# Kernel tuning notes

Measured on AMD Instinct MI355X. Metric: run time of the kernel, lower is better.

## Reference

```python
import jax, jax.numpy as jnp
import numpy as np

B, T, C = 2, 2048, 2048
N_HEADS, N_KV_HEADS = 16, 4
HEAD_DIM = C // N_HEADS  # 128
NUM_GROUPS = N_HEADS // N_KV_HEADS  # 4


def setup_inputs() -> dict:
    key = jax.random.key(0)
    ks = jax.random.split(key, 5)
    s = 1.0 / np.sqrt(C)
    return {
        "x": jax.random.normal(ks[0], (B, T, C), dtype=jnp.float32),
        "Wq": jax.random.normal(ks[1], (C, N_HEADS * HEAD_DIM), dtype=jnp.float32) * s,
        "Wk": jax.random.normal(ks[2], (C, N_KV_HEADS * HEAD_DIM), dtype=jnp.float32) * s,
        "Wv": jax.random.normal(ks[3], (C, N_KV_HEADS * HEAD_DIM), dtype=jnp.float32) * s,
        "Wo": jax.random.normal(ks[4], (C, C), dtype=jnp.float32) * s,
    }


def _rope_tables(seq_len, head_dim, dtype):
    theta = 1.0 / (10000.0 ** (jnp.arange(0, head_dim, 2, dtype=jnp.float32) / head_dim))
    freqs = jnp.arange(seq_len, dtype=jnp.float32)[:, None] * theta[None, :]  # [T, hd/2]
    cos = jnp.concatenate([jnp.cos(freqs), jnp.cos(freqs)], axis=-1)  # [T, hd]
    sin = jnp.concatenate([jnp.sin(freqs), jnp.sin(freqs)], axis=-1)
    return cos.astype(dtype), sin.astype(dtype)


def _rotate_half(x):
    x1, x2 = jnp.split(x, 2, axis=-1)
    return jnp.concatenate([-x2, x1], axis=-1)


def reference(x, Wq, Wk, Wv, Wo):
    b, t, c = x.shape
    q = (x @ Wq).reshape(b, t, N_HEADS, HEAD_DIM).transpose(0, 2, 1, 3)      # [B,H,T,hd]
    k = (x @ Wk).reshape(b, t, N_KV_HEADS, HEAD_DIM).transpose(0, 2, 1, 3)   # [B,Hkv,T,hd]
    v = (x @ Wv).reshape(b, t, N_KV_HEADS, HEAD_DIM).transpose(0, 2, 1, 3)

    cos, sin = _rope_tables(t, HEAD_DIM, x.dtype)  # [T,hd]
    cos = cos[None, None]  # [1,1,T,hd]
    sin = sin[None, None]
    q = q * cos + _rotate_half(q) * sin
    k = k * cos + _rotate_half(k) * sin

    # GQA: expand kv heads (repeat_interleave along head dim)
    k = jnp.repeat(k, NUM_GROUPS, axis=1)  # [B,H,T,hd]
    v = jnp.repeat(v, NUM_GROUPS, axis=1)

    scale = 1.0 / jnp.sqrt(jnp.asarray(HEAD_DIM, dtype=x.dtype))
    scores = jnp.einsum("bhqd,bhkd->bhqk", q, k) * scale  # [B,H,T,T]
    causal = jnp.tril(jnp.ones((t, t), dtype=bool))
    scores = jnp.where(causal[None, None], scores, jnp.asarray(-jnp.inf, dtype=scores.dtype))
    attn = jax.nn.softmax(scores, axis=-1)
    out = jnp.einsum("bhqk,bhkd->bhqd", attn, v)  # [B,H,T,hd]
    out = out.transpose(0, 2, 1, 3).reshape(b, t, c)
    return out @ Wo
```

## Files before the change

kernel.cpp:

```cpp
#include <hip/hip_runtime.h>
#include <hip/hip_bf16.h>
#include <math.h>
#include <utility>

typedef __hip_bfloat16 bf16;
typedef __attribute__((ext_vector_type(8))) short bf16x8;
typedef __attribute__((ext_vector_type(4))) float floatx4;

__device__ __forceinline__ void async_copy16(const bf16* g, bf16* l) {
    __builtin_amdgcn_global_load_lds(
        (__attribute__((address_space(1))) void*)(void*)g,
        (__attribute__((address_space(3))) void*)(void*)l,
        16, 0, 0);
}

__global__ __launch_bounds__(256) void cast_f32_bf16(const float* __restrict__ in,
                                                     bf16* __restrict__ out, int n4) {
    int i = blockIdx.x * 256 + threadIdx.x;
    if (i >= n4) return;
    float4 v = ((const float4*)in)[i];
    union { ushort4 u; bf16 b[4]; } o;
    o.b[0] = __float2bfloat16(v.x);
    o.b[1] = __float2bfloat16(v.y);
    o.b[2] = __float2bfloat16(v.z);
    o.b[3] = __float2bfloat16(v.w);
    ((ushort4*)out)[i] = o.u;
}

__global__ __launch_bounds__(256) void cast_transpose(const float* __restrict__ in,
                                                      bf16* __restrict__ out, int K, int N) {
    __shared__ float tile[32][33];
    int nb = blockIdx.x * 32, kb = blockIdx.y * 32;
    for (int j = threadIdx.y; j < 32; j += 8)
        tile[j][threadIdx.x] = in[(size_t)(kb + j) * N + nb + threadIdx.x];
    __syncthreads();
    for (int j = threadIdx.y; j < 32; j += 8)
        out[(size_t)(nb + j) * K + kb + threadIdx.x] = __float2bfloat16(tile[threadIdx.x][j]);
}

template <bool OUTF32>
__global__ __launch_bounds__(256) void gemm_bt(const bf16* __restrict__ A,
                                               const bf16* __restrict__ Bt,
                                               void* __restrict__ Cout,
                                               int M, int N, int K) {
    __shared__ bf16 As[128 * 32];
    __shared__ bf16 Bs[128 * 32];
    const int tid = threadIdx.x;
    const int wave = tid >> 6, lane = tid & 63;
    const int c = lane & 15, quad = lane >> 4;
    const int wm = wave >> 1, wn = wave & 1;
    const int mBase = blockIdx.y * 128, nBase = blockIdx.x * 128;

    const int sRow = lane >> 2;
    const int sCol = ((lane & 3) ^ ((lane >> 3) & 3)) << 3;
    const int rdOff = (quad ^ ((c >> 1) & 3)) << 3;
    const bf16* gA = A + (size_t)(mBase + wave * 32 + sRow) * K + sCol;
    const bf16* gB = Bt + (size_t)(nBase + wave * 32 + sRow) * K + sCol;
    bf16* lA = As + wave * 1024;
    bf16* lB = Bs + wave * 1024;

    floatx4 acc[4][4];
#pragma unroll
    for (int mt = 0; mt < 4; mt++)
#pragma unroll
        for (int nt = 0; nt < 4; nt++) acc[mt][nt] = (floatx4){0.f, 0.f, 0.f, 0.f};

    for (int k0 = 0; k0 < K; k0 += 32) {
        async_copy16(gA + k0, lA);
        async_copy16(gA + k0 + 16 * K, lA + 512);
        async_copy16(gB + k0, lB);
        async_copy16(gB + k0 + 16 * K, lB + 512);
        __syncthreads();
        bf16x8 af[4], bfr[4];
#pragma unroll
        for (int mt = 0; mt < 4; mt++)
            af[mt] = *(const bf16x8*)(As + (wm * 64 + mt * 16 + c) * 32 + rdOff);
#pragma unroll
        for (int nt = 0; nt < 4; nt++)
            bfr[nt] = *(const bf16x8*)(Bs + (wn * 64 + nt * 16 + c) * 32 + rdOff);
#pragma unroll
        for (int mt = 0; mt < 4; mt++)
#pragma unroll
            for (int nt = 0; nt < 4; nt++)
                acc[mt][nt] = __builtin_amdgcn_mfma_f32_16x16x32_bf16(af[mt], bfr[nt],
                                                                      acc[mt][nt], 0, 0, 0);
        __syncthreads();
    }
#pragma unroll
    for (int mt = 0; mt < 4; mt++)
#pragma unroll
        for (int nt = 0; nt < 4; nt++)
#pragma unroll
            for (int r = 0; r < 4; r++) {
                int row = mBase + wm * 64 + mt * 16 + quad * 4 + r;
                int col = nBase + wn * 64 + nt * 16 + c;
                if (OUTF32)
                    ((float*)Cout)[(size_t)row * N + col] = acc[mt][nt][r];
                else
                    ((bf16*)Cout)[(size_t)row * N + col] = __float2bfloat16(acc[mt][nt][r]);
            }
}

__global__ __launch_bounds__(256) void rope_kernel(bf16* __restrict__ X, int heads, int rowStride) {
    int idx = blockIdx.x * 256 + threadIdx.x;
    int d = idx & 63;
    int h = (idx >> 6) % heads;
    int row = idx / (heads * 64);
    int t = row & 2047;
    float theta = exp2f(-(float)d * 0.20762050593045827f);
    float ang = (float)t * theta;
    float sv, cv;
    __sincosf(ang, &sv, &cv);
    bf16* p = X + (size_t)row * rowStride + h * 128 + d;
    float x1 = __bfloat162float(p[0]);
    float x2 = __bfloat162float(p[64]);
    p[0]  = __float2bfloat16(x1 * cv - x2 * sv);
    p[64] = __float2bfloat16(x2 * cv + x1 * sv);
}

__global__ __launch_bounds__(256) void vtrans(const bf16* __restrict__ QKV,
                                              bf16* __restrict__ Vtg) {
    __shared__ bf16 tile[32][34];
    const int bh = blockIdx.z;
    const int b = bh >> 2, kvh = bh & 3;
    const int t0 = blockIdx.x * 32, d0 = blockIdx.y * 32;
    const bf16* src = QKV + (size_t)b * 2048 * 3072 + 2560 + kvh * 128;
    for (int j = threadIdx.y; j < 32; j += 8)
        tile[j][threadIdx.x] = src[(size_t)(t0 + j) * 3072 + d0 + threadIdx.x];
    __syncthreads();
    bf16* dst = Vtg + (size_t)bh * 128 * 2048;
    for (int j = threadIdx.y; j < 32; j += 8)
        dst[(size_t)(d0 + j) * 2048 + t0 + threadIdx.x] = tile[threadIdx.x][j];
}

__global__ __launch_bounds__(256, 4) void flash_attn3(const bf16* __restrict__ QKV,
                                                      const bf16* __restrict__ Vtg,
                                                      bf16* __restrict__ AO) {
    const int T = 2048, STR = 3072;
    __shared__ bf16 Ks[4 * 64 * 32];
    __shared__ bf16 Vs[2 * 128 * 32];
    __shared__ bf16 Pl[4][16 * 40];
    const int b = blockIdx.z, h = blockIdx.y;
    const int qtile = 31 - blockIdx.x;
    const int q0 = qtile * 64;
    const int kvh = h >> 2;
    const int tid = threadIdx.x, wave = tid >> 6, lane = tid & 63;
    const int c = lane & 15, quad = lane >> 4;
    const float C2 = 0.12751541717525597f;

    const bf16* Kg = QKV + (size_t)b * T * STR + 2048 + kvh * 128;
    const bf16* Vg = Vtg + (size_t)(b * 4 + kvh) * 128 * 2048;
    const int srow = tid >> 2;
    const int xcol = ((tid & 3) ^ ((tid >> 3) & 3)) << 3;
    const int koff = (quad ^ ((c >> 1) & 3)) << 3;
    bf16* PlW = &Pl[wave][0];

    bf16x8 qf[4];
    {
        const bf16* qp = QKV + ((size_t)b * T + q0 + wave * 16 + c) * STR + h * 128 + quad * 8;
#pragma unroll
        for (int ks = 0; ks < 4; ks++) qf[ks] = *(const bf16x8*)(qp + ks * 32);
        const float t = (float)(q0 + wave * 16 + c);
#pragma unroll
        for (int ks = 0; ks < 2; ks++)
#pragma unroll
            for (int j = 0; j < 8; j++) {
                int d = ks * 32 + quad * 8 + j;
                float theta = exp2f((float)d * -0.20762050593045827f);
                float sv, cv;
                __sincosf(t * theta, &sv, &cv);
                float lo = __bfloat162float(((const bf16*)&qf[ks])[j]);
                float hi = __bfloat162float(((const bf16*)&qf[ks + 2])[j]);
                ((bf16*)&qf[ks])[j]     = __float2bfloat16(lo * cv - hi * sv);
                ((bf16*)&qf[ks + 2])[j] = __float2bfloat16(hi * cv + lo * sv);
            }
    }

    floatx4 accO[8];
#pragma unroll
    for (int nt = 0; nt < 8; nt++) accO[nt] = (floatx4){0.f, 0.f, 0.f, 0.f};
    float lrow[4] = {0.f, 0.f, 0.f, 0.f};

    auto tile = [&](int kt0, auto DIAGC) {
        constexpr bool DIAG = decltype(DIAGC)::value;
#pragma unroll
        for (int it = 0; it < 4; it++) {
            async_copy16(Kg + (size_t)(kt0 + srow) * STR + it * 32 + xcol,
                         Ks + it * 2048 + wave * 512);
            async_copy16(Vg + (size_t)((it & 1) * 64 + srow) * 2048 + kt0 + (it >> 1) * 32 + xcol,
                         Vs + it * 2048 + wave * 512);
        }
        __syncthreads();
        floatx4 sf[4];
#pragma unroll
        for (int nt = 0; nt < 4; nt++) sf[nt] = (floatx4){0.f, 0.f, 0.f, 0.f};
#pragma unroll
        for (int ks = 0; ks < 4; ks++)
#pragma unroll
            for (int nt = 0; nt < 4; nt++) {
                bf16x8 kf = *(const bf16x8*)(Ks + ks * 2048 + (nt * 16 + c) * 32 + koff);
                sf[nt] = __builtin_amdgcn_mfma_f32_16x16x32_bf16(qf[ks], kf, sf[nt], 0, 0, 0);
            }
#pragma unroll
        for (int kc = 0; kc < 2; kc++) {
#pragma unroll
            for (int nt2 = 0; nt2 < 2; nt2++) {
                const int nt = kc * 2 + nt2;
#pragma unroll
                for (int r = 0; r < 4; r++) {
                    float p = exp2f(sf[nt][r] * C2);
                    if (DIAG)
                        if (nt * 16 + c > wave * 16 + quad * 4 + r) p = 0.f;
                    lrow[r] += p;
                    PlW[(quad * 4 + r) * 40 + nt2 * 16 + c] = __float2bfloat16(p);
                }
            }
            asm volatile("s_waitcnt lgkmcnt(0)" ::: "memory");
            bf16x8 pf = *(const bf16x8*)(PlW + c * 40 + quad * 8);
#pragma unroll
            for (int nt = 0; nt < 8; nt++) {
                bf16x8 vf = *(const bf16x8*)(Vs + kc * 4096 + (nt * 16 + c) * 32 + koff);
                accO[nt] = __builtin_amdgcn_mfma_f32_16x16x32_bf16(pf, vf, accO[nt], 0, 0, 0);
            }
            asm volatile("" ::: "memory");
        }
        __syncthreads();
    };

    for (int kt0 = 0; kt0 < q0; kt0 += 64)
        tile(kt0, std::integral_constant<bool, false>{});
    tile(q0, std::integral_constant<bool, true>{});

    float inv[4];
#pragma unroll
    for (int r = 0; r < 4; r++) {
        float s = lrow[r];
        s += __shfl_xor(s, 1);
        s += __shfl_xor(s, 2);
        s += __shfl_xor(s, 4);
        s += __shfl_xor(s, 8);
        inv[r] = 1.0f / s;
    }
    const size_t orow = (size_t)b * T + q0 + wave * 16 + quad * 4;
#pragma unroll
    for (int nt = 0; nt < 8; nt++)
#pragma unroll
        for (int r = 0; r < 4; r++)
            AO[(orow + r) * 2048 + h * 128 + nt * 16 + c] =
                __float2bfloat16(accO[nt][r] * inv[r]);
}

extern "C" void kernel_launch(void* const* d_in, const int* in_sizes, int n_in,
                              void* d_out, int out_size, void* d_ws, size_t ws_size,
                              hipStream_t stream) {
    const float* x  = (const float*)d_in[0];
    const float* Wq = (const float*)d_in[1];
    const float* Wk = (const float*)d_in[2];
    const float* Wv = (const float*)d_in[3];
    const float* Wo = (const float*)d_in[4];

    char* ws = (char*)d_ws;
    bf16* xb  = (bf16*)(ws);
    bf16* Vtg = (bf16*)(ws);
    bf16* Wt  = (bf16*)(ws + 16777216);
    bf16* Wot = (bf16*)(ws + 29360128);
    bf16* QKV = (bf16*)(ws + 37748736);
    bf16* AO  = (bf16*)(ws + 62914560);

    cast_f32_bf16<<<8192, 256, 0, stream>>>(x, xb, 2097152);
    cast_transpose<<<dim3(64, 64), dim3(32, 8), 0, stream>>>(Wq, Wt, 2048, 2048);
    cast_transpose<<<dim3(16, 64), dim3(32, 8), 0, stream>>>(Wk, Wt + 2048 * 2048, 2048, 512);
    cast_transpose<<<dim3(16, 64), dim3(32, 8), 0, stream>>>(Wv, Wt + 2560 * 2048, 2048, 512);
    cast_transpose<<<dim3(64, 64), dim3(32, 8), 0, stream>>>(Wo, Wot, 2048, 2048);

    gemm_bt<false><<<dim3(24, 32), 256, 0, stream>>>(xb, Wt, QKV, 4096, 3072, 2048);

    rope_kernel<<<4096, 256, 0, stream>>>(QKV + 2048, 4, 3072);

    vtrans<<<dim3(64, 4, 8), dim3(32, 8), 0, stream>>>(QKV, Vtg);

    flash_attn3<<<dim3(32, 16, 2), 256, 0, stream>>>(QKV, Vtg, AO);

    gemm_bt<true><<<dim3(16, 32), 256, 0, stream>>>(AO, Wot, d_out, 4096, 2048, 2048);
}
```

Measured before the change: 359.6 us.

## Pair complementary causal query tiles per block to balance work and reuse K/V

```diff
diff --git a/kernel.cpp b/kernel.cpp
--- a/kernel.cpp
+++ b/kernel.cpp
@@ -1,7 +1,6 @@
 #include <hip/hip_runtime.h>
 #include <hip/hip_bf16.h>
 #include <math.h>
-#include <utility>
 
 typedef __hip_bfloat16 bf16;
 typedef __attribute__((ext_vector_type(8))) short bf16x8;
@@ -133,33 +132,37 @@
         dst[(size_t)(d0 + j) * 2048 + t0 + threadIdx.x] = tile[threadIdx.x][j];
 }
 
-__global__ __launch_bounds__(256, 4) void flash_attn3(const bf16* __restrict__ QKV,
+__global__ __launch_bounds__(256, 2) void flash_attn4(const bf16* __restrict__ QKV,
                                                       const bf16* __restrict__ Vtg,
                                                       bf16* __restrict__ AO) {
     const int T = 2048, STR = 3072;
     __shared__ bf16 Ks[4 * 64 * 32];
     __shared__ bf16 Vs[2 * 128 * 32];
-    __shared__ bf16 Pl[4][16 * 40];
-    const int b = blockIdx.z, h = blockIdx.y;
-    const int qtile = 31 - blockIdx.x;
-    const int q0 = qtile * 64;
+    __shared__ bf16 Pl[4][2][16 * 40];
+    const int b = blockIdx.z, h = blockIdx.y, pj = blockIdx.x;
     const int kvh = h >> 2;
     const int tid = threadIdx.x, wave = tid >> 6, lane = tid & 63;
     const int c = lane & 15, quad = lane >> 4;
     const float C2 = 0.12751541717525597f;
+
+    const int q0A = (31 - pj) * 64;
+    const int q0B = pj * 64;
 
     const bf16* Kg = QKV + (size_t)b * T * STR + 2048 + kvh * 128;
     const bf16* Vg = Vtg + (size_t)(b * 4 + kvh) * 128 * 2048;
     const int srow = tid >> 2;
     const int xcol = ((tid & 3) ^ ((tid >> 3) & 3)) << 3;
     const int koff = (quad ^ ((c >> 1) & 3)) << 3;
-    bf16* PlW = &Pl[wave][0];
-
-    bf16x8 qf[4];
-    {
+
+    bf16x8 qf[2][4];
+    floatx4 accO[2][8];
+    float lrow[2][4];
+#pragma unroll
+    for (int ph = 0; ph < 2; ph++) {
+        const int q0 = ph ? q0B : q0A;
         const bf16* qp = QKV + ((size_t)b * T + q0 + wave * 16 + c) * STR + h * 128 + quad * 8;
 #pragma unroll
-        for (int ks = 0; ks < 4; ks++) qf[ks] = *(const bf16x8*)(qp + ks * 32);
+        for (int ks = 0; ks < 4; ks++) qf[ph][ks] = *(const bf16x8*)(qp + ks * 32);
         const float t = (float)(q0 + wave * 16 + c);
 #pragma unroll
         for (int ks = 0; ks < 2; ks++)
@@ -169,20 +172,53 @@
                 float theta = exp2f((float)d * -0.20762050593045827f);
                 float sv, cv;
                 __sincosf(t * theta, &sv, &cv);
-                float lo = __bfloat162float(((const bf16*)&qf[ks])[j]);
-                float hi = __bfloat162float(((const bf16*)&qf[ks + 2])[j]);
-                ((bf16*)&qf[ks])[j]     = __float2bfloat16(lo * cv - hi * sv);
-                ((bf16*)&qf[ks + 2])[j] = __float2bfloat16(hi * cv + lo * sv);
-            }
-    }
-
-    floatx4 accO[8];
-#pragma unroll
-    for (int nt = 0; nt < 8; nt++) accO[nt] = (floatx4){0.f, 0.f, 0.f, 0.f};
-    float lrow[4] = {0.f, 0.f, 0.f, 0.f};
-
-    auto tile = [&](int kt0, auto DIAGC) {
-        constexpr bool DIAG = decltype(DIAGC)::value;
+                float lo = __bfloat162float(((const bf16*)&qf[ph][ks])[j]);
+                float hi = __bfloat162float(((const bf16*)&qf[ph][ks + 2])[j]);
+                ((bf16*)&qf[ph][ks])[j]     = __float2bfloat16(lo * cv - hi * sv);
+                ((bf16*)&qf[ph][ks + 2])[j] = __float2bfloat16(hi * cv + lo * sv);
+            }
+#pragma unroll
+        for (int nt = 0; nt < 8; nt++) accO[ph][nt] = (floatx4){0.f, 0.f, 0.f, 0.f};
+#pragma unroll
+        for (int r = 0; r < 4; r++) lrow[ph][r] = 0.f;
+    }
+
+    auto compute = [&](int ph, bool diag) {
+        floatx4 sf[4];
+#pragma unroll
+        for (int nt = 0; nt < 4; nt++) sf[nt] = (floatx4){0.f, 0.f, 0.f, 0.f};
+#pragma unroll
+        for (int ks = 0; ks < 4; ks++)
+#pragma unroll
+            for (int nt = 0; nt < 4; nt++) {
+                bf16x8 kf = *(const bf16x8*)(Ks + ks * 2048 + (nt * 16 + c) * 32 + koff);
+                sf[nt] = __builtin_amdgcn_mfma_f32_16x16x32_bf16(qf[ph][ks], kf, sf[nt], 0, 0, 0);
+            }
+        const int lim = diag ? (wave * 16 + quad * 4) : 1000;
+#pragma unroll
+        for (int kc = 0; kc < 2; kc++) {
+            bf16* PlW = &Pl[wave][kc][0];
+#pragma unroll
+            for (int nt2 = 0; nt2 < 2; nt2++) {
+                const int nt = kc * 2 + nt2;
+#pragma unroll
+                for (int r = 0; r < 4; r++) {
+                    float p = exp2f(sf[nt][r] * C2);
+                    if (nt * 16 + c > lim + r) p = 0.f;
+                    lrow[ph][r] += p;
+                    PlW[(quad * 4 + r) * 40 + nt2 * 16 + c] = __float2bfloat16(p);
+                }
+            }
+            bf16x8 pf = *(const bf16x8*)(PlW + c * 40 + quad * 8);
+#pragma unroll
+            for (int nt = 0; nt < 8; nt++) {
+                bf16x8 vf = *(const bf16x8*)(Vs + kc * 4096 + (nt * 16 + c) * 32 + koff);
+                accO[ph][nt] = __builtin_amdgcn_mfma_f32_16x16x32_bf16(pf, vf, accO[ph][nt], 0, 0, 0);
+            }
+        }
+    };
+
+    for (int kt0 = 0; kt0 <= q0A; kt0 += 64) {
 #pragma unroll
         for (int it = 0; it < 4; it++) {
             async_copy16(Kg + (size_t)(kt0 + srow) * STR + it * 32 + xcol,
@@ -191,63 +227,32 @@
                          Vs + it * 2048 + wave * 512);
         }
         __syncthreads();
-        floatx4 sf[4];
-#pragma unroll
-        for (int nt = 0; nt < 4; nt++) sf[nt] = (floatx4){0.f, 0.f, 0.f, 0.f};
-#pragma unroll
-        for (int ks = 0; ks < 4; ks++)
-#pragma unroll
-            for (int nt = 0; nt < 4; nt++) {
-                bf16x8 kf = *(const bf16x8*)(Ks + ks * 2048 + (nt * 16 + c) * 32 + koff);
-                sf[nt] = __builtin_amdgcn_mfma_f32_16x16x32_bf16(qf[ks], kf, sf[nt], 0, 0, 0);
-            }
-#pragma unroll
-        for (int kc = 0; kc < 2; kc++) {
-#pragma unroll
-            for (int nt2 = 0; nt2 < 2; nt2++) {
-                const int nt = kc * 2 + nt2;
-#pragma unroll
-                for (int r = 0; r < 4; r++) {
-                    float p = exp2f(sf[nt][r] * C2);
-                    if (DIAG)
-                        if (nt * 16 + c > wave * 16 + quad * 4 + r) p = 0.f;
-                    lrow[r] += p;
-                    PlW[(quad * 4 + r) * 40 + nt2 * 16 + c] = __float2bfloat16(p);
-                }
-            }
-            asm volatile("s_waitcnt lgkmcnt(0)" ::: "memory");
-            bf16x8 pf = *(const bf16x8*)(PlW + c * 40 + quad * 8);
-#pragma unroll
-            for (int nt = 0; nt < 8; nt++) {
-                bf16x8 vf = *(const bf16x8*)(Vs + kc * 4096 + (nt * 16 + c) * 32 + koff);
-                accO[nt] = __builtin_amdgcn_mfma_f32_16x16x32_bf16(pf, vf, accO[nt], 0, 0, 0);
-            }
-            asm volatile("" ::: "memory");
+        compute(0, kt0 == q0A);
+        if (kt0 <= q0B) compute(1, kt0 == q0B);
+        __syncthreads();
+    }
+
+#pragma unroll
+    for (int ph = 0; ph < 2; ph++) {
+        const int q0 = ph ? q0B : q0A;
+        float inv[4];
+#pragma unroll
+        for (int r = 0; r < 4; r++) {
+            float s = lrow[ph][r];
+            s += __shfl_xor(s, 1);
+            s += __shfl_xor(s, 2);
+            s += __shfl_xor(s, 4);
+            s += __shfl_xor(s, 8);
+            inv[r] = 1.0f / s;
         }
-        __syncthreads();
-    };
-
-    for (int kt0 = 0; kt0 < q0; kt0 += 64)
-        tile(kt0, std::integral_constant<bool, false>{});
-    tile(q0, std::integral_constant<bool, true>{});
-
-    float inv[4];
-#pragma unroll
-    for (int r = 0; r < 4; r++) {
-        float s = lrow[r];
-        s += __shfl_xor(s, 1);
-        s += __shfl_xor(s, 2);
-        s += __shfl_xor(s, 4);
-        s += __shfl_xor(s, 8);
-        inv[r] = 1.0f / s;
-    }
-    const size_t orow = (size_t)b * T + q0 + wave * 16 + quad * 4;
-#pragma unroll
-    for (int nt = 0; nt < 8; nt++)
-#pragma unroll
-        for (int r = 0; r < 4; r++)
-            AO[(orow + r) * 2048 + h * 128 + nt * 16 + c] =
-                __float2bfloat16(accO[nt][r] * inv[r]);
+        const size_t orow = (size_t)b * T + q0 + wave * 16 + quad * 4;
+#pragma unroll
+        for (int nt = 0; nt < 8; nt++)
+#pragma unroll
+            for (int r = 0; r < 4; r++)
+                AO[(orow + r) * 2048 + h * 128 + nt * 16 + c] =
+                    __float2bfloat16(accO[ph][nt][r] * inv[r]);
+    }
 }
 
 extern "C" void kernel_launch(void* const* d_in, const int* in_sizes, int n_in,
@@ -279,7 +284,7 @@
 
     vtrans<<<dim3(64, 4, 8), dim3(32, 8), 0, stream>>>(QKV, Vtg);
 
-    flash_attn3<<<dim3(32, 16, 2), 256, 0, stream>>>(QKV, Vtg, AO);
+    flash_attn4<<<dim3(16, 16, 2), 256, 0, stream>>>(QKV, Vtg, AO);
 
     gemm_bt<true><<<dim3(16, 32), 256, 0, stream>>>(AO, Wot, d_out, 4096, 2048, 2048);
 }
```

After: 345.7 us. 3.9% less time.

## Balance causal attention work by pairing query tiles and merging split partials

Applied to the files above, without the earlier changes.

```diff
diff --git a/kernel.cpp b/kernel.cpp
--- a/kernel.cpp
+++ b/kernel.cpp
@@ -1,7 +1,6 @@
 #include <hip/hip_runtime.h>
 #include <hip/hip_bf16.h>
 #include <math.h>
-#include <utility>
 
 typedef __hip_bfloat16 bf16;
 typedef __attribute__((ext_vector_type(8))) short bf16x8;
@@ -133,16 +132,17 @@
         dst[(size_t)(d0 + j) * 2048 + t0 + threadIdx.x] = tile[threadIdx.x][j];
 }
 
-__global__ __launch_bounds__(256, 4) void flash_attn3(const bf16* __restrict__ QKV,
+__global__ __launch_bounds__(256, 4) void flash_attn5(const bf16* __restrict__ QKV,
                                                       const bf16* __restrict__ Vtg,
-                                                      bf16* __restrict__ AO) {
+                                                      bf16* __restrict__ Slot0,
+                                                      bf16* __restrict__ Slot1,
+                                                      float* __restrict__ Ls) {
     const int T = 2048, STR = 3072;
     __shared__ bf16 Ks[4 * 64 * 32];
     __shared__ bf16 Vs[2 * 128 * 32];
     __shared__ bf16 Pl[4][16 * 40];
     const int b = blockIdx.z, h = blockIdx.y;
-    const int qtile = 31 - blockIdx.x;
-    const int q0 = qtile * 64;
+    const int pj = blockIdx.x >> 1, s = blockIdx.x & 1;
     const int kvh = h >> 2;
     const int tid = threadIdx.x, wave = tid >> 6, lane = tid & 63;
     const int c = lane & 15, quad = lane >> 4;
@@ -154,100 +154,140 @@
     const int xcol = ((tid & 3) ^ ((tid >> 3) & 3)) << 3;
     const int koff = (quad ^ ((c >> 1) & 3)) << 3;
     bf16* PlW = &Pl[wave][0];
-
-    bf16x8 qf[4];
-    {
-        const bf16* qp = QKV + ((size_t)b * T + q0 + wave * 16 + c) * STR + h * 128 + quad * 8;
-#pragma unroll
-        for (int ks = 0; ks < 4; ks++) qf[ks] = *(const bf16x8*)(qp + ks * 32);
-        const float t = (float)(q0 + wave * 16 + c);
-#pragma unroll
-        for (int ks = 0; ks < 2; ks++)
-#pragma unroll
-            for (int j = 0; j < 8; j++) {
-                int d = ks * 32 + quad * 8 + j;
-                float theta = exp2f((float)d * -0.20762050593045827f);
-                float sv, cv;
-                __sincosf(t * theta, &sv, &cv);
-                float lo = __bfloat162float(((const bf16*)&qf[ks])[j]);
-                float hi = __bfloat162float(((const bf16*)&qf[ks + 2])[j]);
-                ((bf16*)&qf[ks])[j]     = __float2bfloat16(lo * cv - hi * sv);
-                ((bf16*)&qf[ks + 2])[j] = __float2bfloat16(hi * cv + lo * sv);
+    const int qa = 31 - pj;
+
+    auto run_part = [&](int qtile, int ktlo, int kthi, bf16* slot, int lsSlot) {
+        const int q0 = qtile * 64;
+        bf16x8 qf[4];
+        {
+            const bf16* qp = QKV + ((size_t)b * T + q0 + wave * 16 + c) * STR + h * 128 + quad * 8;
+#pragma unroll
+            for (int ks = 0; ks < 4; ks++) qf[ks] = *(const bf16x8*)(qp + ks * 32);
+            const float t = (float)(q0 + wave * 16 + c);
+#pragma unroll
+            for (int ks = 0; ks < 2; ks++)
+#pragma unroll
+                for (int j = 0; j < 8; j++) {
+                    int d = ks * 32 + quad * 8 + j;
+                    float theta = exp2f((float)d * -0.20762050593045827f);
+                    float sv, cv;
+                    __sincosf(t * theta, &sv, &cv);
+                    float lo = __bfloat162float(((const bf16*)&qf[ks])[j]);
+                    float hi = __bfloat162float(((const bf16*)&qf[ks + 2])[j]);
+                    ((bf16*)&qf[ks])[j]     = __float2bfloat16((lo * cv - hi * sv) * C2);
+                    ((bf16*)&qf[ks + 2])[j] = __float2bfloat16((hi * cv + lo * sv) * C2);
+                }
+        }
+        floatx4 accO[8];
+#pragma unroll
+        for (int nt = 0; nt < 8; nt++) accO[nt] = (floatx4){0.f, 0.f, 0.f, 0.f};
+        float lrow[4] = {0.f, 0.f, 0.f, 0.f};
+
+        for (int kt = ktlo; kt < kthi; kt++) {
+            const int kt0 = kt * 64;
+#pragma unroll
+            for (int it = 0; it < 4; it++) {
+                async_copy16(Kg + (size_t)(kt0 + srow) * STR + it * 32 + xcol,
+                             Ks + it * 2048 + wave * 512);
+                async_copy16(Vg + (size_t)((it & 1) * 64 + srow) * 2048 + kt0 + (it >> 1) * 32 + xcol,
+                             Vs + it * 2048 + wave * 512);
             }
+            __syncthreads();
+            floatx4 sf[4];
+#pragma unroll
+            for (int nt = 0; nt < 4; nt++) sf[nt] = (floatx4){0.f, 0.f, 0.f, 0.f};
+#pragma unroll
+            for (int ks = 0; ks < 4; ks++)
+#pragma unroll
+                for (int nt = 0; nt < 4; nt++) {
+                    bf16x8 kf = *(const bf16x8*)(Ks + ks * 2048 + (nt * 16 + c) * 32 + koff);
+                    sf[nt] = __builtin_amdgcn_mfma_f32_16x16x32_bf16(qf[ks], kf, sf[nt], 0, 0, 0);
+                }
+            const int lim = (kt == qtile) ? (wave * 16 + quad * 4) : 1000;
+#pragma unroll
+            for (int kc = 0; kc < 2; kc++) {
+#pragma unroll
+                for (int nt2 = 0; nt2 < 2; nt2++) {
+                    const int nt = kc * 2 + nt2;
+#pragma unroll
+                    for (int r = 0; r < 4; r++) {
+                        float p = exp2f(sf[nt][r]);
+                        if (nt * 16 + c > lim + r) p = 0.f;
+                        lrow[r] += p;
+                        PlW[(quad * 4 + r) * 40 + nt2 * 16 + c] = __float2bfloat16(p);
+                    }
+                }
+                asm volatile("s_waitcnt lgkmcnt(0)" ::: "memory");
+                bf16x8 pf = *(const bf16x8*)(PlW + c * 40 + quad * 8);
+#pragma unroll
+                for (int nt = 0; nt < 8; nt++) {
+                    bf16x8 vf = *(const bf16x8*)(Vs + kc * 4096 + (nt * 16 + c) * 32 + koff);
+                    accO[nt] = __builtin_amdgcn_mfma_f32_16x16x32_bf16(pf, vf, accO[nt], 0, 0, 0);
+                }
+                asm volatile("" ::: "memory");
+            }
+            __syncthreads();
+        }
+        float sred[4];
+#pragma unroll
+        for (int r = 0; r < 4; r++) {
+            float v = lrow[r];
+            v += __shfl_xor(v, 1);
+            v += __shfl_xor(v, 2);
+            v += __shfl_xor(v, 4);
+            v += __shfl_xor(v, 8);
+            sred[r] = v;
+        }
+        if (c == 0) {
+#pragma unroll
+            for (int r = 0; r < 4; r++)
+                Ls[(size_t)lsSlot * 65536 + ((size_t)(b * 16 + h) * 32 + qtile) * 64
+                   + wave * 16 + quad * 4 + r] = sred[r];
+        }
+        const size_t orow = (size_t)b * T + q0 + wave * 16 + quad * 4;
+#pragma unroll
+        for (int nt = 0; nt < 8; nt++)
+#pragma unroll
+            for (int r = 0; r < 4; r++)
+                slot[(orow + r) * 2048 + h * 128 + nt * 16 + c] =
+                    __float2bfloat16(accO[nt][r]);
+    };
+
+    if (s == 0) {
+        run_part(qa, 0, 17, Slot0, 0);
+    } else {
+        run_part(qa, 17, 32 - pj, Slot1, 1);
+        run_part(pj, 0, pj + 1, Slot0, 0);
     }
-
-    floatx4 accO[8];
-#pragma unroll
-    for (int nt = 0; nt < 8; nt++) accO[nt] = (floatx4){0.f, 0.f, 0.f, 0.f};
-    float lrow[4] = {0.f, 0.f, 0.f, 0.f};
-
-    auto tile = [&](int kt0, auto DIAGC) {
-        constexpr bool DIAG = decltype(DIAGC)::value;
-#pragma unroll
-        for (int it = 0; it < 4; it++) {
-            async_copy16(Kg + (size_t)(kt0 + srow) * STR + it * 32 + xcol,
-                         Ks + it * 2048 + wave * 512);
-            async_copy16(Vg + (size_t)((it & 1) * 64 + srow) * 2048 + kt0 + (it >> 1) * 32 + xcol,
-                         Vs + it * 2048 + wave * 512);
-        }
-        __syncthreads();
-        floatx4 sf[4];
-#pragma unroll
-        for (int nt = 0; nt < 4; nt++) sf[nt] = (floatx4){0.f, 0.f, 0.f, 0.f};
-#pragma unroll
-        for (int ks = 0; ks < 4; ks++)
-#pragma unroll
-            for (int nt = 0; nt < 4; nt++) {
-                bf16x8 kf = *(const bf16x8*)(Ks + ks * 2048 + (nt * 16 + c) * 32 + koff);
-                sf[nt] = __builtin_amdgcn_mfma_f32_16x16x32_bf16(qf[ks], kf, sf[nt], 0, 0, 0);
-            }
-#pragma unroll
-        for (int kc = 0; kc < 2; kc++) {
-#pragma unroll
-            for (int nt2 = 0; nt2 < 2; nt2++) {
-                const int nt = kc * 2 + nt2;
-#pragma unroll
-                for (int r = 0; r < 4; r++) {
-                    float p = exp2f(sf[nt][r] * C2);
-                    if (DIAG)
-                        if (nt * 16 + c > wave * 16 + quad * 4 + r) p = 0.f;
-                    lrow[r] += p;
-                    PlW[(quad * 4 + r) * 40 + nt2 * 16 + c] = __float2bfloat16(p);
-                }
-            }
-            asm volatile("s_waitcnt lgkmcnt(0)" ::: "memory");
-            bf16x8 pf = *(const bf16x8*)(PlW + c * 40 + quad * 8);
-#pragma unroll
-            for (int nt = 0; nt < 8; nt++) {
-                bf16x8 vf = *(const bf16x8*)(Vs + kc * 4096 + (nt * 16 + c) * 32 + koff);
-                accO[nt] = __builtin_amdgcn_mfma_f32_16x16x32_bf16(pf, vf, accO[nt], 0, 0, 0);
-            }
-            asm volatile("" ::: "memory");
-        }
-        __syncthreads();
-    };
-
-    for (int kt0 = 0; kt0 < q0; kt0 += 64)
-        tile(kt0, std::integral_constant<bool, false>{});
-    tile(q0, std::integral_constant<bool, true>{});
-
-    float inv[4];
-#pragma unroll
-    for (int r = 0; r < 4; r++) {
-        float s = lrow[r];
-        s += __shfl_xor(s, 1);
-        s += __shfl_xor(s, 2);
-        s += __shfl_xor(s, 4);
-        s += __shfl_xor(s, 8);
-        inv[r] = 1.0f / s;
+}
+
+__global__ __launch_bounds__(256) void attn_merge(bf16* __restrict__ AO,
+                                                  const bf16* __restrict__ P1,
+                                                  const float* __restrict__ Ls) {
+    int i = blockIdx.x * 256 + threadIdx.x;
+    int row = i >> 8;
+    int cg = (i & 255) << 3;
+    int b = row >> 11, t = row & 2047;
+    int qtile = t >> 6;
+    int h = cg >> 7;
+    size_t off = (size_t)row * 2048 + cg;
+    size_t li = ((size_t)(b * 16 + h) * 32 + qtile) * 64 + (t & 63);
+    bf16x8 a0 = *(const bf16x8*)(AO + off);
+    float l = Ls[li];
+    float acc[8];
+#pragma unroll
+    for (int j = 0; j < 8; j++) acc[j] = __bfloat162float(((const bf16*)&a0)[j]);
+    if (qtile >= 16) {
+        bf16x8 a1 = *(const bf16x8*)(P1 + off);
+        l += Ls[65536 + li];
+#pragma unroll
+        for (int j = 0; j < 8; j++) acc[j] += __bfloat162float(((const bf16*)&a1)[j]);
     }
-    const size_t orow = (size_t)b * T + q0 + wave * 16 + quad * 4;
-#pragma unroll
-    for (int nt = 0; nt < 8; nt++)
-#pragma unroll
-        for (int r = 0; r < 4; r++)
-            AO[(orow + r) * 2048 + h * 128 + nt * 16 + c] =
-                __float2bfloat16(accO[nt][r] * inv[r]);
+    float inv = 1.0f / l;
+    bf16x8 o;
+#pragma unroll
+    for (int j = 0; j < 8; j++) ((bf16*)&o)[j] = __float2bfloat16(acc[j] * inv);
+    *(bf16x8*)(AO + off) = o;
 }
 
 extern "C" void kernel_launch(void* const* d_in, const int* in_sizes, int n_in,
@@ -260,12 +300,14 @@
     const float* Wo = (const float*)d_in[4];
 
     char* ws = (char*)d_ws;
-    bf16* xb  = (bf16*)(ws);
-    bf16* Vtg = (bf16*)(ws);
-    bf16* Wt  = (bf16*)(ws + 16777216);
-    bf16* Wot = (bf16*)(ws + 29360128);
-    bf16* QKV = (bf16*)(ws + 37748736);
-    bf16* AO  = (bf16*)(ws + 62914560);
+    bf16* xb   = (bf16*)(ws);
+    bf16* Vtg  = (bf16*)(ws);
+    bf16* Slt1 = (bf16*)(ws + 4194304);
+    float* Ls  = (float*)(ws + 20971520);
+    bf16* Wt   = (bf16*)(ws + 16777216);
+    bf16* Wot  = (bf16*)(ws + 29360128);
+    bf16* QKV  = (bf16*)(ws + 37748736);
+    bf16* AO   = (bf16*)(ws + 62914560);
 
     cast_f32_bf16<<<8192, 256, 0, stream>>>(x, xb, 2097152);
     cast_transpose<<<dim3(64, 64), dim3(32, 8), 0, stream>>>(Wq, Wt, 2048, 2048);
@@ -279,7 +321,9 @@
 
     vtrans<<<dim3(64, 4, 8), dim3(32, 8), 0, stream>>>(QKV, Vtg);
 
-    flash_attn3<<<dim3(32, 16, 2), 256, 0, stream>>>(QKV, Vtg, AO);
+    flash_attn5<<<dim3(32, 16, 2), 256, 0, stream>>>(QKV, Vtg, AO, Slt1, Ls);
+
+    attn_merge<<<4096, 256, 0, stream>>>(AO, Slt1, Ls);
 
     gemm_bt<true><<<dim3(16, 32), 256, 0, stream>>>(AO, Wot, d_out, 4096, 2048, 2048);
 }
```

Result: faster. 326.1 us (-9.3%).
